# Optimization experiments

Hardware: AMD Instinct MI355X
Metric: run time of the kernel (lower is better)

## Reference

```python
import jax, jax.numpy as jnp
import numpy as np

T, D_IN, D_OUT, L, R = 8192, 4096, 4096, 8, 16

def setup_inputs() -> dict:
    key = jax.random.key(0)
    ks = jax.random.split(key, 7)
    x = jax.random.normal(ks[0], (T, D_IN), dtype=jnp.float32)
    W_base = jax.random.normal(ks[1], (D_OUT, D_IN), dtype=jnp.float32) * (1.0 / np.sqrt(D_IN))
    b_base = jax.random.normal(ks[2], (D_OUT,), dtype=jnp.float32) * 0.02
    WA = jax.random.normal(ks[3], (L, R, D_IN), dtype=jnp.float32) * (1.0 / np.sqrt(D_IN))
    WB = jax.random.normal(ks[4], (L, D_OUT, R), dtype=jnp.float32) * 0.02
    scaling = jax.random.uniform(ks[5], (L,), dtype=jnp.float32, minval=0.5, maxval=2.0)
    # contiguous segments of tokens routed to adapters (repeat_interleave(lora_ids, lora_len))
    token_lora = jnp.sort(jax.random.randint(ks[6], (T,), 0, L)).astype(jnp.int32)
    return {"x": x, "W_base": W_base, "b_base": b_base, "WA": WA, "WB": WB,
            "scaling": scaling, "token_lora": token_lora}

def reference(x, W_base, b_base, WA, WB, scaling, token_lora):
    # Base linear: result = base_layer(x)
    base = jnp.einsum('td,od->to', x, W_base) + b_base  # [T, D_OUT]
    # Grouped low-rank GEMM (add_lora): per-token adapter selection via one-hot
    # (avoids materializing per-token [T, R, D_IN] gathered weights).
    onehot = jax.nn.one_hot(token_lora, WA.shape[0], dtype=x.dtype)  # [T, L]
    u = jnp.einsum('td,lrd->tlr', x, WA)            # [T, L, R] (small: L*R << D)
    u_sel = jnp.einsum('tlr,tl->tr', u, onehot)     # [T, R] per-token x @ A_l^T
    v = jnp.einsum('tr,lor,tl->to', u_sel, WB, onehot)  # [T, D_OUT] per-token B_l u
    # per-segment scaling: repeat_interleave(scaling[lora_ids], lora_len)
    out = base + scaling[token_lora][:, None] * v
    return out
```

## Files before the change

### kernel.cpp

```cpp
#include <hip/hip_runtime.h>

#define TT    8192
#define DI    4096
#define DOUT  4096
#define LLORA 8
#define RLORA 16

typedef __bf16 bf16;
typedef __attribute__((ext_vector_type(8))) __bf16 bf16x8;
typedef __attribute__((ext_vector_type(4))) __bf16 bf16x4;
typedef __attribute__((ext_vector_type(4))) float  f32x4;

static const size_t XB_OFF  = 0;
static const size_t WKB_OFF = (size_t)TT * DI * 2;
static const size_t WAB_OFF = WKB_OFF + (size_t)DOUT * DI * 2;
static const size_t U_OFF   = WAB_OFF + (size_t)LLORA * RLORA * DI * 2;

__device__ __forceinline__ void gload_lds16(const bf16* g, bf16* l) {
    __builtin_amdgcn_global_load_lds(
        (const __attribute__((address_space(1))) void*)g,
        (__attribute__((address_space(3))) void*)l,
        16, 0, 0);
}

__global__ __launch_bounds__(256) void convert_w(
    const float* __restrict__ W, const float* __restrict__ WA,
    bf16* __restrict__ wkb, bf16* __restrict__ wab)
{
    const int NW4 = (DOUT * DI) / 4;
    const int NA4 = (LLORA * RLORA * DI) / 4;
    int idx = blockIdx.x * 256 + threadIdx.x;
    int stride = gridDim.x * 256;
    for (int i = idx; i < NW4 + NA4; i += stride) {
        f32x4 v;
        if (i < NW4) v = ((const f32x4*)W)[i];
        else         v = ((const f32x4*)WA)[i - NW4];
        bf16x4 h;
        h[0] = (bf16)v[0]; h[1] = (bf16)v[1]; h[2] = (bf16)v[2]; h[3] = (bf16)v[3];
        if (i < NW4) ((bf16x4*)wkb)[i] = h;
        else         ((bf16x4*)wab)[i - NW4] = h;
    }
}

__global__ __launch_bounds__(256) void prep_x_u(
    const float* __restrict__ x, const bf16* __restrict__ wab,
    const float* __restrict__ scaling, const int* __restrict__ tl,
    bf16* __restrict__ xb, float* __restrict__ u)
{
    __shared__ bf16 sA[128 * 64];
    __shared__ bf16 sB[128 * 64];
    const int bid = blockIdx.x;
    const int bm = bid >> 2, kb = bid & 3;
    const int t0 = bm * 128;
    const int tid  = threadIdx.x;
    const int lane = tid & 63;
    const int wv = tid >> 6;
    const int wr = wv >> 1, wc = wv & 1;

    f32x4 acc[4][4] = {};

    for (int kt = 0; kt < 16; ++kt) {
        const int k = kb * 1024 + kt * 64;
#pragma unroll
        for (int j = 0; j < 8; ++j) {
            int c = j * 256 + tid;
            int row = c >> 4, cf4 = c & 15;
            f32x4 v = *(const f32x4*)(x + (size_t)(t0 + row) * DI + k + cf4 * 4);
            bf16x4 h;
            h[0] = (bf16)v[0]; h[1] = (bf16)v[1]; h[2] = (bf16)v[2]; h[3] = (bf16)v[3];
            *(bf16x4*)(xb + (size_t)(t0 + row) * DI + k + cf4 * 4) = h;
            int byte = row * 128 + ((cf4 * 8) ^ ((row & 7) << 4));
            *(bf16x4*)((char*)sA + byte) = h;
        }
#pragma unroll
        for (int j = 0; j < 4; ++j) {
            int ci = j * 256 + tid;
            int row = ci >> 3;
            int sl = (ci & 7) ^ (row & 7);
            gload_lds16(wab + (size_t)row * DI + k + sl * 8, sB + ci * 8);
        }
        __syncthreads();
#pragma unroll
        for (int ks = 0; ks < 2; ++ks) {
            bf16x8 af[4], bg[4];
#pragma unroll
            for (int mi = 0; mi < 4; ++mi) {
                int row = wr * 64 + mi * 16 + (lane & 15);
                int byte = row * 128 + (((ks * 64) + (lane >> 4) * 16) ^ ((row & 7) << 4));
                af[mi] = *(const bf16x8*)((const char*)sA + byte);
            }
#pragma unroll
            for (int ni = 0; ni < 4; ++ni) {
                int row = wc * 64 + ni * 16 + (lane & 15);
                int byte = row * 128 + (((ks * 64) + (lane >> 4) * 16) ^ ((row & 7) << 4));
                bg[ni] = *(const bf16x8*)((const char*)sB + byte);
            }
#pragma unroll
            for (int mi = 0; mi < 4; ++mi)
#pragma unroll
                for (int ni = 0; ni < 4; ++ni)
                    acc[mi][ni] = __builtin_amdgcn_mfma_f32_16x16x32_bf16(
                        af[mi], bg[ni], acc[mi][ni], 0, 0, 0);
        }
        __syncthreads();
    }

    const int qw = lane >> 4, cl = lane & 15;
#pragma unroll
    for (int mi = 0; mi < 4; ++mi) {
#pragma unroll
        for (int rr = 0; rr < 4; ++rr) {
            int t = t0 + wr * 64 + mi * 16 + qw * 4 + rr;
            int lt = tl[t];
            float s = scaling[lt];
#pragma unroll
            for (int ni = 0; ni < 4; ++ni) {
                int lr = wc * 64 + ni * 16 + cl;
                if ((lr >> 4) == lt)
                    atomicAdd(&u[t * RLORA + (lr & 15)], s * acc[mi][ni][rr]);
            }
        }
    }
}

__global__ __launch_bounds__(256) void gemm_main(
    const bf16* __restrict__ xb, const bf16* __restrict__ wkb,
    const float* __restrict__ bb, const float* __restrict__ WBw,
    const float* __restrict__ u, const int* __restrict__ tl,
    float* __restrict__ out)
{
    __shared__ bf16 smem[32768];
    const int bid = blockIdx.x;
    const int wg = (bid & 7) * 256 + (bid >> 3);
    const int bm = wg >> 5, bn = wg & 31;
    const int brow = bm * 128, bcol = bn * 128;
    const int tid  = threadIdx.x;
    const int lane = tid & 63;
    const int wv = tid >> 6;
    const int wr = wv >> 1, wc = wv & 1;

    f32x4 acc[4][4] = {};

    const bf16* asrc[4];
    const bf16* bsrc[4];
#pragma unroll
    for (int j = 0; j < 4; ++j) {
        int ci = j * 256 + tid;
        int row = ci >> 3;
        int sl = (ci & 7) ^ (row & 7);
        asrc[j] = xb  + (size_t)(brow + row) * DI + sl * 8;
        bsrc[j] = wkb + (size_t)(bcol + row) * DI + sl * 8;
    }

    auto stage = [&](int d, int kt) {
        bf16* sa = smem + d * 8192;
        bf16* sb = smem + 16384 + d * 8192;
#pragma unroll
        for (int j = 0; j < 4; ++j)
            gload_lds16(asrc[j] + kt * 64, sa + (j * 256 + tid) * 8);
#pragma unroll
        for (int j = 0; j < 4; ++j)
            gload_lds16(bsrc[j] + kt * 64, sb + (j * 256 + tid) * 8);
    };

    auto compute = [&](int d) {
        const char* sa = (const char*)(smem + d * 8192);
        const char* sb = (const char*)(smem + 16384 + d * 8192);
#pragma unroll
        for (int ks = 0; ks < 2; ++ks) {
            bf16x8 af[4], bg[4];
#pragma unroll
            for (int mi = 0; mi < 4; ++mi) {
                int row = wr * 64 + mi * 16 + (lane & 15);
                int byte = row * 128 + (((ks * 64) + (lane >> 4) * 16) ^ ((row & 7) << 4));
                af[mi] = *(const bf16x8*)(sa + byte);
            }
#pragma unroll
            for (int ni = 0; ni < 4; ++ni) {
                int row = wc * 64 + ni * 16 + (lane & 15);
                int byte = row * 128 + (((ks * 64) + (lane >> 4) * 16) ^ ((row & 7) << 4));
                bg[ni] = *(const bf16x8*)(sb + byte);
            }
#pragma unroll
            for (int mi = 0; mi < 4; ++mi)
#pragma unroll
                for (int ni = 0; ni < 4; ++ni)
                    acc[mi][ni] = __builtin_amdgcn_mfma_f32_16x16x32_bf16(
                        af[mi], bg[ni], acc[mi][ni], 0, 0, 0);
        }
    };

    stage(0, 0);
    __syncthreads();
    for (int kt = 0; kt < 64; kt += 2) {
        stage(1, kt + 1);
        compute(0);
        __syncthreads();
        if (kt + 2 < 64) stage(0, kt + 2);
        compute(1);
        __syncthreads();
    }

    float* uld = (float*)smem;
    int*   tld = (int*)(smem + 4096);
    {
        const f32x4* ug = (const f32x4*)(u + (size_t)brow * RLORA);
        f32x4* us = (f32x4*)uld;
        us[tid]       = ug[tid];
        us[256 + tid] = ug[256 + tid];
        if (tid < 128) tld[tid] = tl[brow + tid];
    }
    __syncthreads();
    const int luni = (tld[0] == tld[127]) ? tld[0] : -1;
    const int qw = lane >> 4, cl = lane & 15;

    int   ocol[4];
    float bv[4];
#pragma unroll
    for (int ni = 0; ni < 4; ++ni) {
        ocol[ni] = bcol + wc * 64 + ni * 16 + cl;
        bv[ni] = bb[ocol[ni]];
    }
    f32x4 wbv[4][4];
    if (luni >= 0) {
#pragma unroll
        for (int ni = 0; ni < 4; ++ni) {
            const f32x4* wp = (const f32x4*)(WBw + ((size_t)luni * DOUT + ocol[ni]) * RLORA);
#pragma unroll
            for (int j = 0; j < 4; ++j) wbv[ni][j] = wp[j];
        }
    }

#pragma unroll
    for (int mi = 0; mi < 4; ++mi) {
#pragma unroll
        for (int rr = 0; rr < 4; ++rr) {
            int t_loc = wr * 64 + mi * 16 + qw * 4 + rr;
            const float* uv = uld + t_loc * 16;
            int lt = (luni >= 0) ? luni : tld[t_loc];
            float* op = out + (size_t)(brow + t_loc) * DOUT;
#pragma unroll
            for (int ni = 0; ni < 4; ++ni) {
                f32x4 w0, w1, w2, w3;
                if (luni >= 0) {
                    w0 = wbv[ni][0]; w1 = wbv[ni][1]; w2 = wbv[ni][2]; w3 = wbv[ni][3];
                } else {
                    const f32x4* wp = (const f32x4*)(WBw + ((size_t)lt * DOUT + ocol[ni]) * RLORA);
                    w0 = wp[0]; w1 = wp[1]; w2 = wp[2]; w3 = wp[3];
                }
                float dot = 0.f;
#pragma unroll
                for (int r = 0; r < 4; ++r)
                    dot += uv[r] * w0[r] + uv[4 + r] * w1[r]
                         + uv[8 + r] * w2[r] + uv[12 + r] * w3[r];
                op[ocol[ni]] = acc[mi][ni][rr] + bv[ni] + dot;
            }
        }
    }
}

extern "C" void kernel_launch(void* const* d_in, const int* in_sizes, int n_in,
                              void* d_out, int out_size, void* d_ws, size_t ws_size,
                              hipStream_t stream) {
    const float* x   = (const float*)d_in[0];
    const float* W   = (const float*)d_in[1];
    const float* bb  = (const float*)d_in[2];
    const float* WA  = (const float*)d_in[3];
    const float* WBw = (const float*)d_in[4];
    const float* sc  = (const float*)d_in[5];
    const int*   tl  = (const int*)d_in[6];
    float* out = (float*)d_out;

    char* ws = (char*)d_ws;
    bf16*  xb  = (bf16*)(ws + XB_OFF);
    bf16*  wkb = (bf16*)(ws + WKB_OFF);
    bf16*  wab = (bf16*)(ws + WAB_OFF);
    float* u   = (float*)(ws + U_OFF);

    hipMemsetAsync(u, 0, (size_t)TT * RLORA * sizeof(float), stream);
    convert_w<<<2048, 256, 0, stream>>>(W, WA, wkb, wab);
    prep_x_u<<<256, 256, 0, stream>>>(x, wab, sc, tl, xb, u);
    gemm_main<<<2048, 256, 0, stream>>>(xb, wkb, bb, WBw, u, tl, out);
}
```

Baseline: 799.3 us.

## Use 256x256 tiles with 8 waves and finer-grained pipelined staging in main GEMM

New measurement: 722.4 us. 9.6% less time.

```diff
diff --git a/kernel.cpp b/kernel.cpp
--- a/kernel.cpp
+++ b/kernel.cpp
@@ -5,6 +5,7 @@
 #define DOUT  4096
 #define LLORA 8
 #define RLORA 16
+#define NKT   64
 
 typedef __bf16 bf16;
 typedef __attribute__((ext_vector_type(8))) __bf16 bf16x8;
@@ -50,7 +51,7 @@
     __shared__ bf16 sA[128 * 64];
     __shared__ bf16 sB[128 * 64];
     const int bid = blockIdx.x;
-    const int bm = bid >> 2, kb = bid & 3;
+    const int bm = bid >> 3, kb = bid & 7;
     const int t0 = bm * 128;
     const int tid  = threadIdx.x;
     const int lane = tid & 63;
@@ -59,8 +60,8 @@
 
     f32x4 acc[4][4] = {};
 
-    for (int kt = 0; kt < 16; ++kt) {
-        const int k = kb * 1024 + kt * 64;
+    for (int kt = 0; kt < 8; ++kt) {
+        const int k = kb * 512 + kt * 64;
 #pragma unroll
         for (int j = 0; j < 8; ++j) {
             int c = j * 256 + tid;
@@ -123,102 +124,123 @@
     }
 }
 
-__global__ __launch_bounds__(256) void gemm_main(
+__global__ __launch_bounds__(512, 2) void gemm_main(
     const bf16* __restrict__ xb, const bf16* __restrict__ wkb,
     const float* __restrict__ bb, const float* __restrict__ WBw,
     const float* __restrict__ u, const int* __restrict__ tl,
     float* __restrict__ out)
 {
-    __shared__ bf16 smem[32768];
-    const int bid = blockIdx.x;
-    const int wg = (bid & 7) * 256 + (bid >> 3);
-    const int bm = wg >> 5, bn = wg & 31;
-    const int brow = bm * 128, bcol = bn * 128;
+    __shared__ bf16 smem[65536];
     const int tid  = threadIdx.x;
     const int lane = tid & 63;
-    const int wv = tid >> 6;
-    const int wr = wv >> 1, wc = wv & 1;
-
-    f32x4 acc[4][4] = {};
-
-    const bf16* asrc[4];
-    const bf16* bsrc[4];
-#pragma unroll
-    for (int j = 0; j < 4; ++j) {
-        int ci = j * 256 + tid;
-        int row = ci >> 3;
-        int sl = (ci & 7) ^ (row & 7);
-        asrc[j] = xb  + (size_t)(brow + row) * DI + sl * 8;
-        bsrc[j] = wkb + (size_t)(bcol + row) * DI + sl * 8;
-    }
-
-    auto stage = [&](int d, int kt) {
-        bf16* sa = smem + d * 8192;
-        bf16* sb = smem + 16384 + d * 8192;
-#pragma unroll
-        for (int j = 0; j < 4; ++j)
-            gload_lds16(asrc[j] + kt * 64, sa + (j * 256 + tid) * 8);
-#pragma unroll
-        for (int j = 0; j < 4; ++j)
-            gload_lds16(bsrc[j] + kt * 64, sb + (j * 256 + tid) * 8);
-    };
-
-    auto compute = [&](int d) {
-        const char* sa = (const char*)(smem + d * 8192);
-        const char* sb = (const char*)(smem + 16384 + d * 8192);
-#pragma unroll
-        for (int ks = 0; ks < 2; ++ks) {
-            bf16x8 af[4], bg[4];
-#pragma unroll
-            for (int mi = 0; mi < 4; ++mi) {
-                int row = wr * 64 + mi * 16 + (lane & 15);
-                int byte = row * 128 + (((ks * 64) + (lane >> 4) * 16) ^ ((row & 7) << 4));
-                af[mi] = *(const bf16x8*)(sa + byte);
-            }
-#pragma unroll
-            for (int ni = 0; ni < 4; ++ni) {
-                int row = wc * 64 + ni * 16 + (lane & 15);
-                int byte = row * 128 + (((ks * 64) + (lane >> 4) * 16) ^ ((row & 7) << 4));
-                bg[ni] = *(const bf16x8*)(sb + byte);
-            }
+    const int wv   = tid >> 6;
+    const int wr = wv >> 2, wc = wv & 3;
+    const int l15 = lane & 15, hi4 = lane >> 4, l7 = lane & 7;
+
+    int s = (blockIdx.x & 7) * 64 + (blockIdx.x >> 3);
+    const int bn = s >> 5, bm = s & 31;
+    const int brow = bm * 256, bcol = bn * 256;
+
+    const bf16* gA = xb  + (size_t)brow * DI;
+    const bf16* gB = wkb + (size_t)bcol * DI;
+
+    f32x4 acc[8][4] = {};
+    bf16x8 afr[4][2], bfr[4][2];
+
+    auto STAGE = [&](int buf, int isA, int half, int kt) {
+        const bf16* g = isA ? gA : gB;
+        bf16* l = smem + (isA ? 0 : 32768) + buf * 16384 + half * 8192;
+#pragma unroll
+        for (int j = 0; j < 2; ++j) {
+            int chunk = j * 512 + tid;
+            int r = chunk >> 3, sl = chunk & 7;
+            gload_lds16(g + (size_t)(half * 128 + r) * DI + kt * 64 + ((sl ^ (r & 7)) * 8),
+                        l + chunk * 8);
+        }
+    };
+    auto READ_A = [&](int buf, int mh) {
+        const char* base = (const char*)smem + buf * 32768 + (wr * 128 + l15) * 128;
+#pragma unroll
+        for (int mi = 0; mi < 4; ++mi)
+#pragma unroll
+            for (int kk = 0; kk < 2; ++kk)
+                afr[mi][kk] = *(const bf16x8*)(base + (mh * 4 + mi) * 2048 +
+                                  (((kk * 4 + hi4) ^ l7) * 16));
+    };
+    auto READ_B = [&](int buf, int nh) {
+        const char* base = (const char*)smem + 65536 + buf * 32768 + (wc * 64 + l15) * 128;
+#pragma unroll
+        for (int ni = 0; ni < 2; ++ni)
+#pragma unroll
+            for (int kk = 0; kk < 2; ++kk)
+                bfr[nh * 2 + ni][kk] = *(const bf16x8*)(base + (nh * 2 + ni) * 2048 +
+                                  (((kk * 4 + hi4) ^ l7) * 16));
+    };
+    auto MFMA_Q = [&](int mh, int nh) {
+        __builtin_amdgcn_s_setprio(1);
+#pragma unroll
+        for (int kk = 0; kk < 2; ++kk)
 #pragma unroll
             for (int mi = 0; mi < 4; ++mi)
 #pragma unroll
-                for (int ni = 0; ni < 4; ++ni)
-                    acc[mi][ni] = __builtin_amdgcn_mfma_f32_16x16x32_bf16(
-                        af[mi], bg[ni], acc[mi][ni], 0, 0, 0);
-        }
-    };
-
-    stage(0, 0);
-    __syncthreads();
-    for (int kt = 0; kt < 64; kt += 2) {
-        stage(1, kt + 1);
-        compute(0);
-        __syncthreads();
-        if (kt + 2 < 64) stage(0, kt + 2);
-        compute(1);
-        __syncthreads();
+                for (int ni = 0; ni < 2; ++ni)
+                    acc[mh * 4 + mi][nh * 2 + ni] = __builtin_amdgcn_mfma_f32_16x16x32_bf16(
+                        afr[mi][kk], bfr[nh * 2 + ni][kk], acc[mh * 4 + mi][nh * 2 + ni], 0, 0, 0);
+        __builtin_amdgcn_s_setprio(0);
+    };
+
+    auto TILE = [&](int D, int T) {
+        READ_A(D, 0); READ_B(D, 0);
+        if (T + 1 < NKT) STAGE(D ^ 1, 1, 0, T + 1);
+        __builtin_amdgcn_s_barrier();
+        MFMA_Q(0, 0);
+        __builtin_amdgcn_s_barrier();
+        READ_B(D, 1);
+        if (T + 1 < NKT) STAGE(D ^ 1, 1, 1, T + 1);
+        __builtin_amdgcn_s_barrier();
+        MFMA_Q(0, 1);
+        __builtin_amdgcn_s_barrier();
+        READ_A(D, 1);
+        if (T + 2 < NKT) STAGE(D, 0, 0, T + 2);
+        __builtin_amdgcn_s_barrier();
+        MFMA_Q(1, 1);
+        __builtin_amdgcn_s_barrier();
+        if (T + 2 < NKT) STAGE(D, 0, 1, T + 2);
+        if (T < NKT - 2) { asm volatile("s_waitcnt vmcnt(4)" ::: "memory"); }
+        else             { asm volatile("s_waitcnt vmcnt(0)" ::: "memory"); }
+        __builtin_amdgcn_s_barrier();
+        MFMA_Q(1, 0);
+        __builtin_amdgcn_s_barrier();
+    };
+
+    STAGE(0, 0, 0, 0); STAGE(0, 0, 1, 0); STAGE(0, 1, 0, 0); STAGE(0, 1, 1, 0);
+    STAGE(1, 0, 0, 1); STAGE(1, 0, 1, 1);
+    asm volatile("s_waitcnt vmcnt(4)" ::: "memory");
+    __builtin_amdgcn_s_barrier();
+
+#pragma unroll 1
+    for (int tt = 0; tt < NKT; tt += 2) {
+        TILE(0, tt);
+        TILE(1, tt + 1);
     }
 
     float* uld = (float*)smem;
-    int*   tld = (int*)(smem + 4096);
+    int*   tld = (int*)((char*)smem + 16384);
     {
         const f32x4* ug = (const f32x4*)(u + (size_t)brow * RLORA);
         f32x4* us = (f32x4*)uld;
         us[tid]       = ug[tid];
-        us[256 + tid] = ug[256 + tid];
-        if (tid < 128) tld[tid] = tl[brow + tid];
+        us[512 + tid] = ug[512 + tid];
+        if (tid < 256) tld[tid] = tl[brow + tid];
     }
     __syncthreads();
-    const int luni = (tld[0] == tld[127]) ? tld[0] : -1;
-    const int qw = lane >> 4, cl = lane & 15;
+    const int luni = (tld[0] == tld[255]) ? tld[0] : -1;
 
     int   ocol[4];
     float bv[4];
 #pragma unroll
     for (int ni = 0; ni < 4; ++ni) {
-        ocol[ni] = bcol + wc * 64 + ni * 16 + cl;
+        ocol[ni] = bcol + wc * 64 + ni * 16 + l15;
         bv[ni] = bb[ocol[ni]];
     }
     f32x4 wbv[4][4];
@@ -232,10 +254,10 @@
     }
 
 #pragma unroll
-    for (int mi = 0; mi < 4; ++mi) {
+    for (int mi = 0; mi < 8; ++mi) {
 #pragma unroll
         for (int rr = 0; rr < 4; ++rr) {
-            int t_loc = wr * 64 + mi * 16 + qw * 4 + rr;
+            int t_loc = wr * 128 + mi * 16 + hi4 * 4 + rr;
             const float* uv = uld + t_loc * 16;
             int lt = (luni >= 0) ? luni : tld[t_loc];
             float* op = out + (size_t)(brow + t_loc) * DOUT;
@@ -279,6 +301,6 @@
 
     hipMemsetAsync(u, 0, (size_t)TT * RLORA * sizeof(float), stream);
     convert_w<<<2048, 256, 0, stream>>>(W, WA, wkb, wab);
-    prep_x_u<<<256, 256, 0, stream>>>(x, wab, sc, tl, xb, u);
-    gemm_main<<<2048, 256, 0, stream>>>(xb, wkb, bb, WBw, u, tl, out);
-}
+    prep_x_u<<<512, 256, 0, stream>>>(x, wab, sc, tl, xb, u);
+    gemm_main<<<512, 512, 0, stream>>>(xb, wkb, bb, WBw, u, tl, out);
+}
```
